# Kernel tuning notes

Measured on AMD Instinct MI355X. Metric: run time of the kernel, lower is better.

The kernel has to match this reference:

```python
import jax, jax.numpy as jnp
import numpy as np


def _grid_sample(feat, grid):
    """Bilinear grid_sample, zeros padding, align_corners=False (torch default).
    feat: (B,C,H,W); grid: (B,Hg,Wg,2) normalized to [-1,1]. Returns (B,C,Hg,Wg)."""
    B, C, H, W = feat.shape
    gx, gy = grid[..., 0], grid[..., 1]
    ix = ((gx + 1.0) * W - 1.0) * 0.5
    iy = ((gy + 1.0) * H - 1.0) * 0.5
    x0 = jnp.floor(ix)
    y0 = jnp.floor(iy)
    wx = ix - x0
    wy = iy - y0

    def sample_one(f, x0, y0, wx, wy):
        def gather(xi, yi):
            valid = (xi >= 0) & (xi <= W - 1) & (yi >= 0) & (yi <= H - 1)
            xc = jnp.clip(xi, 0, W - 1).astype(jnp.int32)
            yc = jnp.clip(yi, 0, H - 1).astype(jnp.int32)
            return f[:, yc, xc] * valid[None].astype(f.dtype)
        v00 = gather(x0, y0)
        v01 = gather(x0 + 1, y0)
        v10 = gather(x0, y0 + 1)
        v11 = gather(x0 + 1, y0 + 1)
        return (v00 * (1 - wx) * (1 - wy) + v01 * wx * (1 - wy)
                + v10 * (1 - wx) * wy + v11 * wx * wy)

    return jax.vmap(sample_one)(feat, x0, y0, wx, wy)


def _homo_warp(src_feat, depth_hypo, src_K, src_c2w, ref_K, ref_c2w):
    """src_feat (B,C,H,W), depth_hypo (B,D,H,W) -> warped (B,C,D,H,W)."""
    B, C, H, W = src_feat.shape
    D = depth_hypo.shape[1]
    src_w2c = jnp.linalg.inv(src_c2w)
    ref_w2c = jnp.linalg.inv(ref_c2w)
    # Faithful to torch: clone w2c, overwrite top-left 3x3 with intrinsics.
    src_K4 = src_w2c.at[:, :3, :3].set(src_K)
    ref_K4 = ref_w2c.at[:, :3, :3].set(ref_K)
    src_proj = src_K4 @ src_w2c
    ref_proj = ref_K4 @ ref_w2c
    proj = src_proj @ jnp.linalg.inv(ref_proj)
    rot = proj[:, :3, :3]                      # (B,3,3)
    trans = proj[:, :3, 3]                     # (B,3)
    y, x = jnp.meshgrid(jnp.arange(H, dtype=src_feat.dtype),
                        jnp.arange(W, dtype=src_feat.dtype), indexing='ij')
    xyz = jnp.stack([x.ravel(), y.ravel(), jnp.ones(H * W, src_feat.dtype)], 0)  # (3,HW)
    rot_xyz = jnp.einsum('bij,jn->bin', rot, xyz)                                 # (B,3,HW)
    d = depth_hypo.reshape(B, 1, D, H * W)
    proj_xyz = rot_xyz[:, :, None, :] * d + trans[:, :, None, None]               # (B,3,D,HW)
    proj_xy = proj_xyz[:, :2] / proj_xyz[:, 2:3]
    gx = proj_xy[:, 0] / ((W - 1) / 2.0) - 1.0
    gy = proj_xy[:, 1] / ((H - 1) / 2.0) - 1.0
    grid = jax.lax.stop_gradient(jnp.stack([gx, gy], -1).reshape(B, D * H, W, 2))
    warped = _grid_sample(src_feat, grid)                                          # (B,C,D*H,W)
    return warped.reshape(B, C, D, H, W)


def _unfold5(x):
    """F.unfold(k=5,p=2) reshaped: (B,C,H,W) -> (B,C,25,H,W); k = dy*5+dx."""
    B, C, H, W = x.shape
    xp = jnp.pad(x, ((0, 0), (0, 0), (2, 2), (2, 2)))
    return jnp.stack([xp[:, :, dy:dy + H, dx:dx + W]
                      for dy in range(5) for dx in range(5)], axis=2)


def _cost_aggregation(cost, ref_feat, depth_hypo):
    B, D, H, W = cost.shape
    CENTER = 12  # index of 5x5 window center
    cost_nb = _unfold5(cost)                                           # (B,D,25,H,W)
    depth_nb = jax.lax.stop_gradient(_unfold5(depth_hypo))             # (B,D,25,H,W)
    w_depth = jax.nn.softmax(-jnp.abs(depth_nb - depth_nb[:, :, CENTER:CENTER + 1]), axis=2)
    feat_nb = jax.lax.stop_gradient(_unfold5(ref_feat))                # (B,C,25,H,W)
    w_feat = jnp.sum(feat_nb[:, :, CENTER:CENTER + 1] * feat_nb, axis=1, keepdims=True)
    w_feat = jax.nn.softmax(jnp.broadcast_to(w_feat, (B, D, 25, H, W)), axis=2)
    weight = jax.lax.stop_gradient(jax.nn.softmax(w_depth * w_feat, axis=2))
    return jnp.sum(cost_nb * weight, axis=2)                           # (B,D,H,W)


def setup_inputs() -> dict:
    key = jax.random.key(0)
    V, B, C, D, H, W = 3, 2, 32, 32, 128, 160
    k1, k2 = jax.random.split(key)
    features = jax.random.normal(k1, (V, B, C, H, W), jnp.float32)
    uncertainty = jax.random.normal(k2, (B, H, W), jnp.float32)
    K = np.array([[float(W), 0.0, (W - 1) / 2.0],
                  [0.0, float(W), (H - 1) / 2.0],
                  [0.0, 0.0, 1.0]], np.float32)
    intrinsics = np.broadcast_to(K, (V, B, 3, 3)).copy()
    c2w = np.tile(np.eye(4, dtype=np.float32), (V, B, 1, 1))
    for v in range(1, V):
        ang = 0.05 * v
        R = np.array([[np.cos(ang), 0.0, np.sin(ang)],
                      [0.0, 1.0, 0.0],
                      [-np.sin(ang), 0.0, np.cos(ang)]], np.float32)
        c2w[v, :, :3, :3] = R
        c2w[v, :, 0, 3] = 0.2 * v
    depth_vals = jnp.asarray(np.linspace(2.0, 10.0, D, dtype=np.float32))
    depth_hypo = jnp.broadcast_to(depth_vals[None, :, None, None], (B, D, H, W)) + 0.0
    return {
        'features': features,
        'intrinsics': jnp.asarray(intrinsics),
        'cam_to_world': jnp.asarray(c2w),
        'depth_hypo': depth_hypo,
        'uncertainty': uncertainty,
    }


def reference(features, intrinsics, cam_to_world, depth_hypo, uncertainty):
    ref_feat = features[0]                                             # (B,C,H,W)
    V = features.shape[0]
    unc = jax.nn.sigmoid(uncertainty)[:, None, None]                   # (B,1,1,H,W)
    pairwise = []
    for v in range(1, V):
        warped = _homo_warp(features[v], depth_hypo,
                            intrinsics[v], cam_to_world[v],
                            intrinsics[0], cam_to_world[0])            # (B,C,D,H,W)
        c = jnp.sum(ref_feat[:, :, None] * warped, axis=1, keepdims=True)  # correlation
        pairwise.append(c * unc)
    cost = jnp.min(jnp.stack(pairwise, 0), axis=0)[:, 0]               # (B,D,H,W)
    agg = _cost_aggregation(cost, ref_feat, depth_hypo)
    prob = jax.nn.softmax(agg, axis=1)
    return jnp.sum(prob * depth_hypo, axis=1)                          # (B,H,W)
```

## Files before the change

### kernel.cpp

```cpp
#include <hip/hip_runtime.h>
#include <hip/hip_fp16.h>
#include <math.h>

#define V_ 3
#define B_ 2
#define C_ 32
#define D_ 32
#define H_ 128
#define W_ 160
#define HW_ (H_*W_)
#define NPIX_ (B_*H_*W_)
#define NCOST_ (B_*D_*H_*W_)

struct H8 { __half2 h[4]; };

__device__ __forceinline__ void inv4(const double* m, double* o) {
    double inv[16];
    inv[0]  =  m[5]*m[10]*m[15] - m[5]*m[11]*m[14] - m[9]*m[6]*m[15] + m[9]*m[7]*m[14] + m[13]*m[6]*m[11] - m[13]*m[7]*m[10];
    inv[4]  = -m[4]*m[10]*m[15] + m[4]*m[11]*m[14] + m[8]*m[6]*m[15] - m[8]*m[7]*m[14] - m[12]*m[6]*m[11] + m[12]*m[7]*m[10];
    inv[8]  =  m[4]*m[9]*m[15]  - m[4]*m[11]*m[13] - m[8]*m[5]*m[15] + m[8]*m[7]*m[13] + m[12]*m[5]*m[11] - m[12]*m[7]*m[9];
    inv[12] = -m[4]*m[9]*m[14]  + m[4]*m[10]*m[13] + m[8]*m[5]*m[14] - m[8]*m[6]*m[13] - m[12]*m[5]*m[10] + m[12]*m[6]*m[9];
    inv[1]  = -m[1]*m[10]*m[15] + m[1]*m[11]*m[14] + m[9]*m[2]*m[15] - m[9]*m[3]*m[14] - m[13]*m[2]*m[11] + m[13]*m[3]*m[10];
    inv[5]  =  m[0]*m[10]*m[15] - m[0]*m[11]*m[14] - m[8]*m[2]*m[15] + m[8]*m[3]*m[14] + m[12]*m[2]*m[11] - m[12]*m[3]*m[10];
    inv[9]  = -m[0]*m[9]*m[15]  + m[0]*m[11]*m[13] + m[8]*m[1]*m[15] - m[8]*m[3]*m[13] - m[12]*m[1]*m[11] + m[12]*m[3]*m[9];
    inv[13] =  m[0]*m[9]*m[14]  - m[0]*m[10]*m[13] - m[8]*m[1]*m[14] + m[8]*m[2]*m[13] + m[12]*m[1]*m[10] - m[12]*m[2]*m[9];
    inv[2]  =  m[1]*m[6]*m[15]  - m[1]*m[7]*m[14]  - m[5]*m[2]*m[15] + m[5]*m[3]*m[14] + m[13]*m[2]*m[7]  - m[13]*m[3]*m[6];
    inv[6]  = -m[0]*m[6]*m[15]  + m[0]*m[7]*m[14]  + m[4]*m[2]*m[15] - m[4]*m[3]*m[14] - m[12]*m[2]*m[7]  + m[12]*m[3]*m[6];
    inv[10] =  m[0]*m[5]*m[15]  - m[0]*m[7]*m[13]  - m[4]*m[1]*m[15] + m[4]*m[3]*m[13] + m[12]*m[1]*m[7]  - m[12]*m[3]*m[5];
    inv[14] = -m[0]*m[5]*m[14]  + m[0]*m[6]*m[13]  + m[4]*m[1]*m[14] - m[4]*m[2]*m[13] - m[12]*m[1]*m[6]  + m[12]*m[2]*m[5];
    inv[3]  = -m[1]*m[6]*m[11]  + m[1]*m[7]*m[10]  + m[5]*m[2]*m[11] - m[5]*m[3]*m[10] - m[9]*m[2]*m[7]   + m[9]*m[3]*m[6];
    inv[7]  =  m[0]*m[6]*m[11]  - m[0]*m[7]*m[10]  - m[4]*m[2]*m[11] + m[4]*m[3]*m[10] + m[8]*m[2]*m[7]   - m[8]*m[3]*m[6];
    inv[11] = -m[0]*m[5]*m[11]  + m[0]*m[7]*m[9]   + m[4]*m[1]*m[11] - m[4]*m[3]*m[9]  - m[8]*m[1]*m[7]   + m[8]*m[3]*m[5];
    inv[15] =  m[0]*m[5]*m[10]  - m[0]*m[6]*m[9]   - m[4]*m[1]*m[10] + m[4]*m[2]*m[9]  + m[8]*m[1]*m[6]   - m[8]*m[2]*m[5];
    double det = m[0]*inv[0] + m[1]*inv[4] + m[2]*inv[8] + m[3]*inv[12];
    det = 1.0 / det;
    for (int i = 0; i < 16; i++) o[i] = inv[i] * det;
}

__device__ __forceinline__ void mm4(const double* A, const double* Bm, double* Cm) {
    for (int r = 0; r < 4; r++)
        for (int c = 0; c < 4; c++) {
            double s = 0.0;
            for (int k = 0; k < 4; k++) s += A[r*4+k] * Bm[k*4+c];
            Cm[r*4+c] = s;
        }
}

__global__ void proj_kernel(const float* __restrict__ K, const float* __restrict__ c2w,
                            float* __restrict__ proj_out) {
    int t = blockIdx.x * blockDim.x + threadIdx.x;
    if (t >= (V_-1) * B_) return;
    int vv = t / B_;
    int b  = t % B_;
    int v  = vv + 1;
    double sc[16], rc[16];
    for (int i = 0; i < 16; i++) {
        sc[i] = (double)c2w[((size_t)v * B_ + b) * 16 + i];
        rc[i] = (double)c2w[((size_t)0 * B_ + b) * 16 + i];
    }
    double sw[16], rw[16];
    inv4(sc, sw);
    inv4(rc, rw);
    double sK[16], rK[16];
    for (int i = 0; i < 16; i++) { sK[i] = sw[i]; rK[i] = rw[i]; }
    for (int r = 0; r < 3; r++)
        for (int c = 0; c < 3; c++) {
            sK[r*4+c] = (double)K[((size_t)v * B_ + b) * 9 + r*3 + c];
            rK[r*4+c] = (double)K[((size_t)0 * B_ + b) * 9 + r*3 + c];
        }
    double sp[16], rp[16], rpi[16], P[16];
    mm4(sK, sw, sp);
    mm4(rK, rw, rp);
    inv4(rp, rpi);
    mm4(sp, rpi, P);
    float* o = proj_out + (size_t)t * 12;
    for (int r = 0; r < 3; r++)
        for (int c = 0; c < 3; c++) o[r*3+c] = (float)P[r*4+c];
    for (int r = 0; r < 3; r++) o[9+r] = (float)P[r*4+3];
}

__global__ void __launch_bounds__(256) transpose_kernel(const float* __restrict__ feat,
                                                        float* __restrict__ refT,
                                                        __half* __restrict__ fh) {
    __shared__ float lds[32][33];
    int bid = blockIdx.x;
    int xt = bid % (W_ / 32);
    int y  = (bid / (W_ / 32)) % H_;
    int vb = bid / ((W_ / 32) * H_);
    int v = vb >> 1, b = vb & 1;
    int x0 = xt * 32;
    int tid = threadIdx.x;
    int xl = tid & 31;
    int ch = tid >> 5;
#pragma unroll
    for (int it = 0; it < 4; it++) {
        int c = it * 8 + ch;
        lds[c][xl] = feat[((size_t)(vb * C_ + c) * H_ + y) * W_ + x0 + xl];
    }
    __syncthreads();
    int c4 = tid & 7;
    int xw = tid >> 3;
    float4 o;
    o.x = lds[c4*4+0][xw];
    o.y = lds[c4*4+1][xw];
    o.z = lds[c4*4+2][xw];
    o.w = lds[c4*4+3][xw];
    size_t pix = (size_t)(b * H_ + y) * W_ + x0 + xw;
    if (v == 0) {
        *(float4*)(refT + pix * C_ + c4 * 4) = o;
    } else {
        uint2 st;
        __half2 p0 = __floats2half2_rn(o.x, o.y);
        __half2 p1 = __floats2half2_rn(o.z, o.w);
        st.x = *(unsigned int*)&p0;
        st.y = *(unsigned int*)&p1;
        size_t dst = ((size_t)((v - 1) * B_ + b) * HW_ + (y * W_ + x0 + xw));
        *(uint2*)((unsigned short*)fh + dst * C_ + c4 * 4) = st;
    }
}

__global__ void __launch_bounds__(256, 4) cost_kernel(const float* __restrict__ refT,
                                                      const __half* __restrict__ fh,
                                                      const float* __restrict__ depth,
                                                      const float* __restrict__ unc,
                                                      const float* __restrict__ proj,
                                                      float* __restrict__ cost) {
    __shared__ float4 lw[2][256];
    __shared__ int4   lo[2][256];
    int tid = threadIdx.x;
    const int blocksPerDt = NPIX_ / 32;
    int dt      = blockIdx.x / blocksPerDt;
    int pixbase = (blockIdx.x % blocksPerDt) * 32;
    int d0 = dt * 8;

    {
        int pixl = tid & 31;
        int dl   = tid >> 5;
        int pix = pixbase + pixl;
        int x = pix % W_;
        int y = (pix / W_) % H_;
        int b = pix / HW_;
        float dep = depth[((b * D_ + d0 + dl) * H_ + y) * W_ + x];
        float fx = (float)x, fy = (float)y;
#pragma unroll
        for (int v = 0; v < 2; v++) {
            const float* P = proj + ((size_t)v * B_ + b) * 12;
            float rx = P[0]*fx + P[1]*fy + P[2];
            float ry = P[3]*fx + P[4]*fy + P[5];
            float rz = P[6]*fx + P[7]*fy + P[8];
            float px = rx * dep + P[9];
            float py = ry * dep + P[10];
            float pz = rz * dep + P[11];
            float inv_pz = 1.0f / pz;
            float t0 = px * inv_pz;
            float t1 = py * inv_pz;
            float gx = t0 / ((W_ - 1) * 0.5f) - 1.0f;
            float gy = t1 / ((H_ - 1) * 0.5f) - 1.0f;
            float ix = ((gx + 1.0f) * W_ - 1.0f) * 0.5f;
            float iy = ((gy + 1.0f) * H_ - 1.0f) * 0.5f;
            float x0f = floorf(ix), y0f = floorf(iy);
            float wx = ix - x0f, wy = iy - y0f;
            int x0 = (int)x0f, y0 = (int)y0f;
            int x1 = x0 + 1, y1 = y0 + 1;
            bool vx0 = (x0 >= 0) && (x0 <= W_ - 1);
            bool vx1 = (x1 >= 0) && (x1 <= W_ - 1);
            bool vy0 = (y0 >= 0) && (y0 <= H_ - 1);
            bool vy1 = (y1 >= 0) && (y1 <= H_ - 1);
            float4 w;
            w.x = (vx0 && vy0) ? (1.0f - wx) * (1.0f - wy) : 0.0f;
            w.y = (vx1 && vy0) ? wx * (1.0f - wy) : 0.0f;
            w.z = (vx0 && vy1) ? (1.0f - wx) * wy : 0.0f;
            w.w = (vx1 && vy1) ? wx * wy : 0.0f;
            int xc0 = min(max(x0, 0), W_ - 1), xc1 = min(max(x1, 0), W_ - 1);
            int yc0 = min(max(y0, 0), H_ - 1), yc1 = min(max(y1, 0), H_ - 1);
            int4 o;
            o.x = yc0 * W_ + xc0;
            o.y = yc0 * W_ + xc1;
            o.z = yc1 * W_ + xc0;
            o.w = yc1 * W_ + xc1;
            lw[v][tid] = w;
            lo[v][tid] = o;
        }
    }
    __syncthreads();

    int c8 = tid & 3;
    int g  = (tid >> 2) & 31;
    int h  = tid >> 7;
    int pix = pixbase + g;
    int x = pix % W_;
    int y = (pix / W_) % H_;
    int b = pix / HW_;

    const float4* rT4 = (const float4*)refT;
    const float4 r0 = rT4[(size_t)pix * 8 + c8 * 2];
    const float4 r1 = rT4[(size_t)pix * 8 + c8 * 2 + 1];
    const H8* fh8 = (const H8*)fh;
    size_t baseA = ((size_t)(0 * B_ + b) * HW_) * 4 + c8;
    size_t baseB = ((size_t)(1 * B_ + b) * HW_) * 4 + c8;

    float u = unc[pix];
    float sig = 1.0f / (1.0f + __expf(-u));

    float myres = 0.0f;
#pragma unroll
    for (int i = 0; i < 4; i++) {
        int e = (h * 4 + i) * 32 + g;
        float pv[2];
#pragma unroll
        for (int v = 0; v < 2; v++) {
            float4 Wt = lw[v][e];
            int4   Of = lo[v][e];
            size_t base = v ? baseB : baseA;
            H8 a  = fh8[base + (size_t)Of.x * 4];
            H8 bq = fh8[base + (size_t)Of.y * 4];
            H8 cq = fh8[base + (size_t)Of.z * 4];
            H8 eq = fh8[base + (size_t)Of.w * 4];
            __half2 w0 = __float2half2_rn(Wt.x);
            __half2 w1 = __float2half2_rn(Wt.y);
            __half2 w2 = __float2half2_rn(Wt.z);
            __half2 w3 = __float2half2_rn(Wt.w);
            __half2 acc0 = __hmul2(w0, a.h[0]);
            __half2 acc1 = __hmul2(w0, a.h[1]);
            __half2 acc2 = __hmul2(w0, a.h[2]);
            __half2 acc3 = __hmul2(w0, a.h[3]);
            acc0 = __hfma2(w1, bq.h[0], acc0);
            acc1 = __hfma2(w1, bq.h[1], acc1);
            acc2 = __hfma2(w1, bq.h[2], acc2);
            acc3 = __hfma2(w1, bq.h[3], acc3);
            acc0 = __hfma2(w2, cq.h[0], acc0);
            acc1 = __hfma2(w2, cq.h[1], acc1);
            acc2 = __hfma2(w2, cq.h[2], acc2);
            acc3 = __hfma2(w2, cq.h[3], acc3);
            acc0 = __hfma2(w3, eq.h[0], acc0);
            acc1 = __hfma2(w3, eq.h[1], acc1);
            acc2 = __hfma2(w3, eq.h[2], acc2);
            acc3 = __hfma2(w3, eq.h[3], acc3);
            float2 f0 = __half22float2(acc0);
            float2 f1 = __half22float2(acc1);
            float2 f2 = __half22float2(acc2);
            float2 f3 = __half22float2(acc3);
            float p = r0.x*f0.x + r0.y*f0.y + r0.z*f1.x + r0.w*f1.y
                    + r1.x*f2.x + r1.y*f2.y + r1.z*f3.x + r1.w*f3.y;
            p += __shfl_xor(p, 1);
            p += __shfl_xor(p, 2);
            pv[v] = p;
        }
        float r = fminf(pv[0], pv[1]) * sig;
        if (c8 == i) myres = r;
    }
    cost[((b * D_ + d0 + h * 4 + c8) * H_ + y) * W_ + x] = myres;
}

__global__ void __launch_bounds__(256) wfeat_kernel(const float* __restrict__ refT,
                                                    float* __restrict__ wfeat) {
    __shared__ float4 wbox[5 * 36 * 8];
    int tid = threadIdx.x;
    int g  = tid >> 3;
    int c4 = tid & 7;
    int pixbase = blockIdx.x * 32;
    int x0 = pixbase % W_;
    int yb = (pixbase / W_) % H_;
    int b  = pixbase / HW_;
    const float4* rT4 = (const float4*)refT;

    for (int e = tid; e < 5 * 36 * 8; e += 256) {
        int ent = e >> 3, q = e & 7;
        int ry = ent / 36, rx = ent - ry * 36;
        int yy = yb + ry - 2, xx = x0 + rx - 2;
        float4 val = make_float4(0.f, 0.f, 0.f, 0.f);
        if (yy >= 0 && yy < H_ && xx >= 0 && xx < W_)
            val = rT4[(size_t)((b * H_ + yy) * W_ + xx) * 8 + q];
        wbox[e] = val;
    }
    __syncthreads();

    const float4 r = wbox[(2 * 36 + g + 2) * 8 + c4];
    float logit[25];
#pragma unroll
    for (int k = 0; k < 25; k++) {
        int dy = k / 5, dx = k % 5;
        float4 q = wbox[(dy * 36 + g + dx) * 8 + c4];
        float p = r.x*q.x + r.y*q.y + r.z*q.z + r.w*q.w;
        p += __shfl_xor(p, 1);
        p += __shfl_xor(p, 2);
        p += __shfl_xor(p, 4);
        logit[k] = p;
    }
    float m = logit[0];
#pragma unroll
    for (int k = 1; k < 25; k++) m = fmaxf(m, logit[k]);
    float s = 0.0f;
#pragma unroll
    for (int k = 0; k < 25; k++) { logit[k] = __expf(logit[k] - m); s += logit[k]; }
    float inv_s = 1.0f / s;
    int pix = pixbase + g;
#pragma unroll
    for (int t = 0; t < 3; t++) {
        int k = c4 + 8 * t;
        wfeat[(size_t)k * NPIX_ + pix] = logit[k] * inv_s;
    }
    if (c4 == 0) wfeat[(size_t)24 * NPIX_ + pix] = logit[24] * inv_s;
}

__global__ void __launch_bounds__(256, 4) agg_kernel(const float* __restrict__ depth,
                                                     const float* __restrict__ cost,
                                                     const float* __restrict__ wfeat,
                                                     float* __restrict__ agg) {
    int tid = threadIdx.x;
    int xl = tid & 31;
    int dl = tid >> 5;
    int bid = blockIdx.x;
    int xt  = bid % (W_ / 32);
    int rem = bid / (W_ / 32);
    int by  = rem % (B_ * H_);
    int dg  = rem / (B_ * H_);
    int y = by % H_;
    int b = by / H_;
    int x = xt * 32 + xl;
    int d = dg * 8 + dl;
    int pix = (b * H_ + y) * W_ + x;
    size_t dslice = (size_t)(b * D_ + d) * HW_;

    float dc = depth[dslice + y * W_ + x];

    float wd[25];
    float m1 = -1e30f;
#pragma unroll
    for (int k = 0; k < 25; k++) {
        int dy = k / 5 - 2, dx = k % 5 - 2;
        int ny = y + dy, nx = x + dx;
        bool ok = (ny >= 0 && ny < H_ && nx >= 0 && nx < W_);
        float nd = ok ? depth[dslice + ny * W_ + nx] : 0.0f;
        float l = -fabsf(nd - dc);
        wd[k] = l;
        m1 = fmaxf(m1, l);
    }
    float s1 = 0.0f;
#pragma unroll
    for (int k = 0; k < 25; k++) { wd[k] = __expf(wd[k] - m1); s1 += wd[k]; }
    float inv_s1 = 1.0f / s1;

    float m2 = -1e30f;
#pragma unroll
    for (int k = 0; k < 25; k++) {
        float l = (wd[k] * inv_s1) * wfeat[(size_t)k * NPIX_ + pix];
        wd[k] = l;
        m2 = fmaxf(m2, l);
    }
    float s2 = 0.0f;
    float acc = 0.0f;
#pragma unroll
    for (int k = 0; k < 25; k++) {
        float e = __expf(wd[k] - m2);
        s2 += e;
        int dy = k / 5 - 2, dx = k % 5 - 2;
        int ny = y + dy, nx = x + dx;
        bool ok = (ny >= 0 && ny < H_ && nx >= 0 && nx < W_);
        float cv = ok ? cost[dslice + ny * W_ + nx] : 0.0f;
        acc += cv * e;
    }
    agg[dslice + y * W_ + x] = acc / s2;
}

__global__ void __launch_bounds__(256) final_kernel(const float* __restrict__ agg,
                                                    const float* __restrict__ depth,
                                                    float* __restrict__ out) {
    int idx = blockIdx.x * 256 + threadIdx.x;
    if (idx >= NPIX_) return;
    int x = idx % W_;
    int y = (idx / W_) % H_;
    int b = idx / (W_ * H_);
    size_t base = ((size_t)(b * D_) * H_ + y) * W_ + x;
    float a[D_];
    float m = -1e30f;
#pragma unroll
    for (int d = 0; d < D_; d++) {
        a[d] = agg[base + (size_t)d * HW_];
        m = fmaxf(m, a[d]);
    }
    float s = 0.0f, ws = 0.0f;
#pragma unroll
    for (int d = 0; d < D_; d++) {
        float e = __expf(a[d] - m);
        s += e;
        ws += e * depth[base + (size_t)d * HW_];
    }
    out[idx] = ws / s;
}

extern "C" void kernel_launch(void* const* d_in, const int* in_sizes, int n_in,
                              void* d_out, int out_size, void* d_ws, size_t ws_size,
                              hipStream_t stream) {
    const float* features = (const float*)d_in[0];
    const float* intr     = (const float*)d_in[1];
    const float* c2w      = (const float*)d_in[2];
    const float* depth    = (const float*)d_in[3];
    const float* unc      = (const float*)d_in[4];
    float* out = (float*)d_out;

    float*  ws    = (float*)d_ws;
    float*  refT  = ws;
    __half* fh    = (__half*)(refT + (size_t)B_ * HW_ * C_);
    float*  cost  = (float*)(fh + (size_t)2 * B_ * HW_ * C_);
    float*  wfeat = cost + NCOST_;
    float*  agg   = wfeat + (size_t)25 * NPIX_;
    float*  proj  = agg + NCOST_;

    hipLaunchKernelGGL(proj_kernel, dim3(1), dim3(64), 0, stream, intr, c2w, proj);
    hipLaunchKernelGGL(transpose_kernel, dim3(V_ * B_ * H_ * (W_ / 32)), dim3(256), 0, stream,
                       features, refT, fh);
    hipLaunchKernelGGL(cost_kernel, dim3((NPIX_ * 4) / 32), dim3(256), 0, stream,
                       refT, fh, depth, unc, proj, cost);
    hipLaunchKernelGGL(wfeat_kernel, dim3(NPIX_ / 32), dim3(256), 0, stream, refT, wfeat);
    hipLaunchKernelGGL(agg_kernel, dim3((W_ / 32) * B_ * H_ * (D_ / 8)), dim3(256), 0, stream,
                       depth, cost, wfeat, agg);
    hipLaunchKernelGGL(final_kernel, dim3(NPIX_ / 256), dim3(256), 0, stream, agg, depth, out);
}
```

Before: 79.16 us.

## Fuse six kernels into three: merge proj, wfeat, and agg+final stages

Folds the projection-matrix computation into an extra block of the transpose kernel and runs the wfeat computation as extra blocks of the cost kernel, which share a shared-memory union. The agg and final softmax kernels become one kernel per row tile of 32 pixels: it handles all 32 depths, stages wfeat in shared memory and reduces over depth in-block, so the agg intermediate buffer is never written. It also drops the max-subtraction in the two inner softmaxes, since the logits are bounded. The aim is to cut launch overhead and global traffic for the agg buffer, at the cost of fewer blocks in the agg stage and a serial 32-thread depth reduction.

Result: faster. 70.02 us (-11.5%).

```diff
diff --git a/kernel.cpp b/kernel.cpp
--- a/kernel.cpp
+++ b/kernel.cpp
@@ -46,50 +46,52 @@
         }
 }
 
-__global__ void proj_kernel(const float* __restrict__ K, const float* __restrict__ c2w,
-                            float* __restrict__ proj_out) {
-    int t = blockIdx.x * blockDim.x + threadIdx.x;
-    if (t >= (V_-1) * B_) return;
-    int vv = t / B_;
-    int b  = t % B_;
-    int v  = vv + 1;
-    double sc[16], rc[16];
-    for (int i = 0; i < 16; i++) {
-        sc[i] = (double)c2w[((size_t)v * B_ + b) * 16 + i];
-        rc[i] = (double)c2w[((size_t)0 * B_ + b) * 16 + i];
-    }
-    double sw[16], rw[16];
-    inv4(sc, sw);
-    inv4(rc, rw);
-    double sK[16], rK[16];
-    for (int i = 0; i < 16; i++) { sK[i] = sw[i]; rK[i] = rw[i]; }
-    for (int r = 0; r < 3; r++)
-        for (int c = 0; c < 3; c++) {
-            sK[r*4+c] = (double)K[((size_t)v * B_ + b) * 9 + r*3 + c];
-            rK[r*4+c] = (double)K[((size_t)0 * B_ + b) * 9 + r*3 + c];
-        }
-    double sp[16], rp[16], rpi[16], P[16];
-    mm4(sK, sw, sp);
-    mm4(rK, rw, rp);
-    inv4(rp, rpi);
-    mm4(sp, rpi, P);
-    float* o = proj_out + (size_t)t * 12;
-    for (int r = 0; r < 3; r++)
-        for (int c = 0; c < 3; c++) o[r*3+c] = (float)P[r*4+c];
-    for (int r = 0; r < 3; r++) o[9+r] = (float)P[r*4+3];
-}
-
-__global__ void __launch_bounds__(256) transpose_kernel(const float* __restrict__ feat,
+__global__ void __launch_bounds__(256) transproj_kernel(const float* __restrict__ feat,
+                                                        const float* __restrict__ K,
+                                                        const float* __restrict__ c2w,
                                                         float* __restrict__ refT,
-                                                        __half* __restrict__ fh) {
+                                                        __half* __restrict__ fh,
+                                                        float* __restrict__ proj_out) {
+    int bid = blockIdx.x;
+    int tid = threadIdx.x;
+    if (bid == V_ * B_ * H_ * (W_ / 32)) {
+        int t = tid;
+        if (t >= (V_-1) * B_) return;
+        int vv = t / B_;
+        int b  = t % B_;
+        int v  = vv + 1;
+        double sc[16], rc[16];
+        for (int i = 0; i < 16; i++) {
+            sc[i] = (double)c2w[((size_t)v * B_ + b) * 16 + i];
+            rc[i] = (double)c2w[((size_t)0 * B_ + b) * 16 + i];
+        }
+        double sw[16], rw[16];
+        inv4(sc, sw);
+        inv4(rc, rw);
+        double sK[16], rK[16];
+        for (int i = 0; i < 16; i++) { sK[i] = sw[i]; rK[i] = rw[i]; }
+        for (int r = 0; r < 3; r++)
+            for (int c = 0; c < 3; c++) {
+                sK[r*4+c] = (double)K[((size_t)v * B_ + b) * 9 + r*3 + c];
+                rK[r*4+c] = (double)K[((size_t)0 * B_ + b) * 9 + r*3 + c];
+            }
+        double sp[16], rp[16], rpi[16], P[16];
+        mm4(sK, sw, sp);
+        mm4(rK, rw, rp);
+        inv4(rp, rpi);
+        mm4(sp, rpi, P);
+        float* o = proj_out + (size_t)t * 12;
+        for (int r = 0; r < 3; r++)
+            for (int c = 0; c < 3; c++) o[r*3+c] = (float)P[r*4+c];
+        for (int r = 0; r < 3; r++) o[9+r] = (float)P[r*4+3];
+        return;
+    }
     __shared__ float lds[32][33];
-    int bid = blockIdx.x;
     int xt = bid % (W_ / 32);
     int y  = (bid / (W_ / 32)) % H_;
     int vb = bid / ((W_ / 32) * H_);
     int v = vb >> 1, b = vb & 1;
     int x0 = xt * 32;
-    int tid = threadIdx.x;
     int xl = tid & 31;
     int ch = tid >> 5;
 #pragma unroll
@@ -119,274 +121,268 @@
     }
 }
 
-__global__ void __launch_bounds__(256, 4) cost_kernel(const float* __restrict__ refT,
-                                                      const __half* __restrict__ fh,
-                                                      const float* __restrict__ depth,
-                                                      const float* __restrict__ unc,
-                                                      const float* __restrict__ proj,
-                                                      float* __restrict__ cost) {
-    __shared__ float4 lw[2][256];
-    __shared__ int4   lo[2][256];
+union SmemU {
+    struct { float4 lw[2][256]; int4 lo[2][256]; } c;
+    float4 wbox[5 * 36 * 8];
+};
+__global__ void __launch_bounds__(256, 4) costwfeat_kernel(const float* __restrict__ refT,
+                                                           const __half* __restrict__ fh,
+                                                           const float* __restrict__ depth,
+                                                           const float* __restrict__ unc,
+                                                           const float* __restrict__ proj,
+                                                           float* __restrict__ cost,
+                                                           float* __restrict__ wfeat) {
+    __shared__ SmemU sm;
     int tid = threadIdx.x;
+    int bid = blockIdx.x;
     const int blocksPerDt = NPIX_ / 32;
-    int dt      = blockIdx.x / blocksPerDt;
-    int pixbase = (blockIdx.x % blocksPerDt) * 32;
-    int d0 = dt * 8;
-
-    {
-        int pixl = tid & 31;
-        int dl   = tid >> 5;
-        int pix = pixbase + pixl;
+
+    if (bid < 4 * blocksPerDt) {
+        int dt      = bid / blocksPerDt;
+        int pixbase = (bid % blocksPerDt) * 32;
+        int d0 = dt * 8;
+        {
+            int pixl = tid & 31;
+            int dl   = tid >> 5;
+            int pix = pixbase + pixl;
+            int x = pix % W_;
+            int y = (pix / W_) % H_;
+            int b = pix / HW_;
+            float dep = depth[((b * D_ + d0 + dl) * H_ + y) * W_ + x];
+            float fx = (float)x, fy = (float)y;
+#pragma unroll
+            for (int v = 0; v < 2; v++) {
+                const float* P = proj + ((size_t)v * B_ + b) * 12;
+                float rx = P[0]*fx + P[1]*fy + P[2];
+                float ry = P[3]*fx + P[4]*fy + P[5];
+                float rz = P[6]*fx + P[7]*fy + P[8];
+                float px = rx * dep + P[9];
+                float py = ry * dep + P[10];
+                float pz = rz * dep + P[11];
+                float inv_pz = 1.0f / pz;
+                float t0 = px * inv_pz;
+                float t1 = py * inv_pz;
+                float gx = t0 / ((W_ - 1) * 0.5f) - 1.0f;
+                float gy = t1 / ((H_ - 1) * 0.5f) - 1.0f;
+                float ix = ((gx + 1.0f) * W_ - 1.0f) * 0.5f;
+                float iy = ((gy + 1.0f) * H_ - 1.0f) * 0.5f;
+                float x0f = floorf(ix), y0f = floorf(iy);
+                float wx = ix - x0f, wy = iy - y0f;
+                int x0 = (int)x0f, y0 = (int)y0f;
+                int x1 = x0 + 1, y1 = y0 + 1;
+                bool vx0 = (x0 >= 0) && (x0 <= W_ - 1);
+                bool vx1 = (x1 >= 0) && (x1 <= W_ - 1);
+                bool vy0 = (y0 >= 0) && (y0 <= H_ - 1);
+                bool vy1 = (y1 >= 0) && (y1 <= H_ - 1);
+                float4 w;
+                w.x = (vx0 && vy0) ? (1.0f - wx) * (1.0f - wy) : 0.0f;
+                w.y = (vx1 && vy0) ? wx * (1.0f - wy) : 0.0f;
+                w.z = (vx0 && vy1) ? (1.0f - wx) * wy : 0.0f;
+                w.w = (vx1 && vy1) ? wx * wy : 0.0f;
+                int xc0 = min(max(x0, 0), W_ - 1), xc1 = min(max(x1, 0), W_ - 1);
+                int yc0 = min(max(y0, 0), H_ - 1), yc1 = min(max(y1, 0), H_ - 1);
+                int4 o;
+                o.x = yc0 * W_ + xc0;
+                o.y = yc0 * W_ + xc1;
+                o.z = yc1 * W_ + xc0;
+                o.w = yc1 * W_ + xc1;
+                sm.c.lw[v][tid] = w;
+                sm.c.lo[v][tid] = o;
+            }
+        }
+        __syncthreads();
+
+        int c8 = tid & 3;
+        int g  = (tid >> 2) & 31;
+        int h  = tid >> 7;
+        int pix = pixbase + g;
         int x = pix % W_;
         int y = (pix / W_) % H_;
         int b = pix / HW_;
-        float dep = depth[((b * D_ + d0 + dl) * H_ + y) * W_ + x];
-        float fx = (float)x, fy = (float)y;
-#pragma unroll
-        for (int v = 0; v < 2; v++) {
-            const float* P = proj + ((size_t)v * B_ + b) * 12;
-            float rx = P[0]*fx + P[1]*fy + P[2];
-            float ry = P[3]*fx + P[4]*fy + P[5];
-            float rz = P[6]*fx + P[7]*fy + P[8];
-            float px = rx * dep + P[9];
-            float py = ry * dep + P[10];
-            float pz = rz * dep + P[11];
-            float inv_pz = 1.0f / pz;
-            float t0 = px * inv_pz;
-            float t1 = py * inv_pz;
-            float gx = t0 / ((W_ - 1) * 0.5f) - 1.0f;
-            float gy = t1 / ((H_ - 1) * 0.5f) - 1.0f;
-            float ix = ((gx + 1.0f) * W_ - 1.0f) * 0.5f;
-            float iy = ((gy + 1.0f) * H_ - 1.0f) * 0.5f;
-            float x0f = floorf(ix), y0f = floorf(iy);
-            float wx = ix - x0f, wy = iy - y0f;
-            int x0 = (int)x0f, y0 = (int)y0f;
-            int x1 = x0 + 1, y1 = y0 + 1;
-            bool vx0 = (x0 >= 0) && (x0 <= W_ - 1);
-            bool vx1 = (x1 >= 0) && (x1 <= W_ - 1);
-            bool vy0 = (y0 >= 0) && (y0 <= H_ - 1);
-            bool vy1 = (y1 >= 0) && (y1 <= H_ - 1);
-            float4 w;
-            w.x = (vx0 && vy0) ? (1.0f - wx) * (1.0f - wy) : 0.0f;
-            w.y = (vx1 && vy0) ? wx * (1.0f - wy) : 0.0f;
-            w.z = (vx0 && vy1) ? (1.0f - wx) * wy : 0.0f;
-            w.w = (vx1 && vy1) ? wx * wy : 0.0f;
-            int xc0 = min(max(x0, 0), W_ - 1), xc1 = min(max(x1, 0), W_ - 1);
-            int yc0 = min(max(y0, 0), H_ - 1), yc1 = min(max(y1, 0), H_ - 1);
-            int4 o;
-            o.x = yc0 * W_ + xc0;
-            o.y = yc0 * W_ + xc1;
-            o.z = yc1 * W_ + xc0;
-            o.w = yc1 * W_ + xc1;
-            lw[v][tid] = w;
-            lo[v][tid] = o;
-        }
-    }
-    __syncthreads();
-
-    int c8 = tid & 3;
-    int g  = (tid >> 2) & 31;
-    int h  = tid >> 7;
-    int pix = pixbase + g;
-    int x = pix % W_;
-    int y = (pix / W_) % H_;
-    int b = pix / HW_;
-
-    const float4* rT4 = (const float4*)refT;
-    const float4 r0 = rT4[(size_t)pix * 8 + c8 * 2];
-    const float4 r1 = rT4[(size_t)pix * 8 + c8 * 2 + 1];
-    const H8* fh8 = (const H8*)fh;
-    size_t baseA = ((size_t)(0 * B_ + b) * HW_) * 4 + c8;
-    size_t baseB = ((size_t)(1 * B_ + b) * HW_) * 4 + c8;
-
-    float u = unc[pix];
-    float sig = 1.0f / (1.0f + __expf(-u));
-
-    float myres = 0.0f;
-#pragma unroll
-    for (int i = 0; i < 4; i++) {
-        int e = (h * 4 + i) * 32 + g;
-        float pv[2];
-#pragma unroll
-        for (int v = 0; v < 2; v++) {
-            float4 Wt = lw[v][e];
-            int4   Of = lo[v][e];
-            size_t base = v ? baseB : baseA;
-            H8 a  = fh8[base + (size_t)Of.x * 4];
-            H8 bq = fh8[base + (size_t)Of.y * 4];
-            H8 cq = fh8[base + (size_t)Of.z * 4];
-            H8 eq = fh8[base + (size_t)Of.w * 4];
-            __half2 w0 = __float2half2_rn(Wt.x);
-            __half2 w1 = __float2half2_rn(Wt.y);
-            __half2 w2 = __float2half2_rn(Wt.z);
-            __half2 w3 = __float2half2_rn(Wt.w);
-            __half2 acc0 = __hmul2(w0, a.h[0]);
-            __half2 acc1 = __hmul2(w0, a.h[1]);
-            __half2 acc2 = __hmul2(w0, a.h[2]);
-            __half2 acc3 = __hmul2(w0, a.h[3]);
-            acc0 = __hfma2(w1, bq.h[0], acc0);
-            acc1 = __hfma2(w1, bq.h[1], acc1);
-            acc2 = __hfma2(w1, bq.h[2], acc2);
-            acc3 = __hfma2(w1, bq.h[3], acc3);
-            acc0 = __hfma2(w2, cq.h[0], acc0);
-            acc1 = __hfma2(w2, cq.h[1], acc1);
-            acc2 = __hfma2(w2, cq.h[2], acc2);
-            acc3 = __hfma2(w2, cq.h[3], acc3);
-            acc0 = __hfma2(w3, eq.h[0], acc0);
-            acc1 = __hfma2(w3, eq.h[1], acc1);
-            acc2 = __hfma2(w3, eq.h[2], acc2);
-            acc3 = __hfma2(w3, eq.h[3], acc3);
-            float2 f0 = __half22float2(acc0);
-            float2 f1 = __half22float2(acc1);
-            float2 f2 = __half22float2(acc2);
-            float2 f3 = __half22float2(acc3);
-            float p = r0.x*f0.x + r0.y*f0.y + r0.z*f1.x + r0.w*f1.y
-                    + r1.x*f2.x + r1.y*f2.y + r1.z*f3.x + r1.w*f3.y;
+
+        const float4* rT4 = (const float4*)refT;
+        const float4 r0 = rT4[(size_t)pix * 8 + c8 * 2];
+        const float4 r1 = rT4[(size_t)pix * 8 + c8 * 2 + 1];
+        const H8* fh8 = (const H8*)fh;
+        size_t baseA = ((size_t)(0 * B_ + b) * HW_) * 4 + c8;
+        size_t baseB = ((size_t)(1 * B_ + b) * HW_) * 4 + c8;
+
+        float u = unc[pix];
+        float sig = 1.0f / (1.0f + __expf(-u));
+
+        float myres = 0.0f;
+#pragma unroll
+        for (int i = 0; i < 4; i++) {
+            int e = (h * 4 + i) * 32 + g;
+            float pv[2];
+#pragma unroll
+            for (int v = 0; v < 2; v++) {
+                float4 Wt = sm.c.lw[v][e];
+                int4   Of = sm.c.lo[v][e];
+                size_t base = v ? baseB : baseA;
+                H8 a  = fh8[base + (size_t)Of.x * 4];
+                H8 bq = fh8[base + (size_t)Of.y * 4];
+                H8 cq = fh8[base + (size_t)Of.z * 4];
+                H8 eq = fh8[base + (size_t)Of.w * 4];
+                __half2 w0 = __float2half2_rn(Wt.x);
+                __half2 w1 = __float2half2_rn(Wt.y);
+                __half2 w2 = __float2half2_rn(Wt.z);
+                __half2 w3 = __float2half2_rn(Wt.w);
+                __half2 acc0 = __hmul2(w0, a.h[0]);
+                __half2 acc1 = __hmul2(w0, a.h[1]);
+                __half2 acc2 = __hmul2(w0, a.h[2]);
+                __half2 acc3 = __hmul2(w0, a.h[3]);
+                acc0 = __hfma2(w1, bq.h[0], acc0);
+                acc1 = __hfma2(w1, bq.h[1], acc1);
+                acc2 = __hfma2(w1, bq.h[2], acc2);
+                acc3 = __hfma2(w1, bq.h[3], acc3);
+                acc0 = __hfma2(w2, cq.h[0], acc0);
+                acc1 = __hfma2(w2, cq.h[1], acc1);
+                acc2 = __hfma2(w2, cq.h[2], acc2);
+                acc3 = __hfma2(w2, cq.h[3], acc3);
+                acc0 = __hfma2(w3, eq.h[0], acc0);
+                acc1 = __hfma2(w3, eq.h[1], acc1);
+                acc2 = __hfma2(w3, eq.h[2], acc2);
+                acc3 = __hfma2(w3, eq.h[3], acc3);
+                float2 f0 = __half22float2(acc0);
+                float2 f1 = __half22float2(acc1);
+                float2 f2 = __half22float2(acc2);
+                float2 f3 = __half22float2(acc3);
+                float p = r0.x*f0.x + r0.y*f0.y + r0.z*f1.x + r0.w*f1.y
+                        + r1.x*f2.x + r1.y*f2.y + r1.z*f3.x + r1.w*f3.y;
+                p += __shfl_xor(p, 1);
+                p += __shfl_xor(p, 2);
+                pv[v] = p;
+            }
+            float r = fminf(pv[0], pv[1]) * sig;
+            if (c8 == i) myres = r;
+        }
+        cost[((b * D_ + d0 + h * 4 + c8) * H_ + y) * W_ + x] = myres;
+    } else {
+        int wbid = bid - 4 * blocksPerDt;
+        int g  = tid >> 3;
+        int c4 = tid & 7;
+        int pixbase = wbid * 32;
+        int x0 = pixbase % W_;
+        int yb = (pixbase / W_) % H_;
+        int b  = pixbase / HW_;
+        const float4* rT4 = (const float4*)refT;
+
+        for (int e = tid; e < 5 * 36 * 8; e += 256) {
+            int ent = e >> 3, q = e & 7;
+            int ry = ent / 36, rx = ent - ry * 36;
+            int yy = yb + ry - 2, xx = x0 + rx - 2;
+            float4 val = make_float4(0.f, 0.f, 0.f, 0.f);
+            if (yy >= 0 && yy < H_ && xx >= 0 && xx < W_)
+                val = rT4[(size_t)((b * H_ + yy) * W_ + xx) * 8 + q];
+            sm.wbox[e] = val;
+        }
+        __syncthreads();
+
+        const float4 r = sm.wbox[(2 * 36 + g + 2) * 8 + c4];
+        float logit[25];
+#pragma unroll
+        for (int k = 0; k < 25; k++) {
+            int dy = k / 5, dx = k % 5;
+            float4 q = sm.wbox[(dy * 36 + g + dx) * 8 + c4];
+            float p = r.x*q.x + r.y*q.y + r.z*q.z + r.w*q.w;
             p += __shfl_xor(p, 1);
             p += __shfl_xor(p, 2);
-            pv[v] = p;
-        }
-        float r = fminf(pv[0], pv[1]) * sig;
-        if (c8 == i) myres = r;
-    }
-    cost[((b * D_ + d0 + h * 4 + c8) * H_ + y) * W_ + x] = myres;
-}
-
-__global__ void __launch_bounds__(256) wfeat_kernel(const float* __restrict__ refT,
-                                                    float* __restrict__ wfeat) {
-    __shared__ float4 wbox[5 * 36 * 8];
-    int tid = threadIdx.x;
-    int g  = tid >> 3;
-    int c4 = tid & 7;
-    int pixbase = blockIdx.x * 32;
-    int x0 = pixbase % W_;
-    int yb = (pixbase / W_) % H_;
-    int b  = pixbase / HW_;
-    const float4* rT4 = (const float4*)refT;
-
-    for (int e = tid; e < 5 * 36 * 8; e += 256) {
-        int ent = e >> 3, q = e & 7;
-        int ry = ent / 36, rx = ent - ry * 36;
-        int yy = yb + ry - 2, xx = x0 + rx - 2;
-        float4 val = make_float4(0.f, 0.f, 0.f, 0.f);
-        if (yy >= 0 && yy < H_ && xx >= 0 && xx < W_)
-            val = rT4[(size_t)((b * H_ + yy) * W_ + xx) * 8 + q];
-        wbox[e] = val;
-    }
-    __syncthreads();
-
-    const float4 r = wbox[(2 * 36 + g + 2) * 8 + c4];
-    float logit[25];
-#pragma unroll
-    for (int k = 0; k < 25; k++) {
-        int dy = k / 5, dx = k % 5;
-        float4 q = wbox[(dy * 36 + g + dx) * 8 + c4];
-        float p = r.x*q.x + r.y*q.y + r.z*q.z + r.w*q.w;
-        p += __shfl_xor(p, 1);
-        p += __shfl_xor(p, 2);
-        p += __shfl_xor(p, 4);
-        logit[k] = p;
-    }
-    float m = logit[0];
-#pragma unroll
-    for (int k = 1; k < 25; k++) m = fmaxf(m, logit[k]);
-    float s = 0.0f;
-#pragma unroll
-    for (int k = 0; k < 25; k++) { logit[k] = __expf(logit[k] - m); s += logit[k]; }
-    float inv_s = 1.0f / s;
-    int pix = pixbase + g;
-#pragma unroll
-    for (int t = 0; t < 3; t++) {
-        int k = c4 + 8 * t;
-        wfeat[(size_t)k * NPIX_ + pix] = logit[k] * inv_s;
-    }
-    if (c4 == 0) wfeat[(size_t)24 * NPIX_ + pix] = logit[24] * inv_s;
-}
-
-__global__ void __launch_bounds__(256, 4) agg_kernel(const float* __restrict__ depth,
-                                                     const float* __restrict__ cost,
-                                                     const float* __restrict__ wfeat,
-                                                     float* __restrict__ agg) {
+            p += __shfl_xor(p, 4);
+            logit[k] = p;
+        }
+        float m = logit[0];
+#pragma unroll
+        for (int k = 1; k < 25; k++) m = fmaxf(m, logit[k]);
+        float s = 0.0f;
+#pragma unroll
+        for (int k = 0; k < 25; k++) { logit[k] = __expf(logit[k] - m); s += logit[k]; }
+        float inv_s = 1.0f / s;
+        int pix = pixbase + g;
+#pragma unroll
+        for (int t = 0; t < 3; t++) {
+            int k = c4 + 8 * t;
+            wfeat[(size_t)k * NPIX_ + pix] = logit[k] * inv_s;
+        }
+        if (c4 == 0) wfeat[(size_t)24 * NPIX_ + pix] = logit[24] * inv_s;
+    }
+}
+
+__global__ void __launch_bounds__(256, 4) aggfinal_kernel(const float* __restrict__ depth,
+                                                          const float* __restrict__ cost,
+                                                          const float* __restrict__ wfeat,
+                                                          float* __restrict__ out) {
+    __shared__ float wf[25][33];
+    __shared__ float aval[D_][33];
+    __shared__ float dval[D_][33];
     int tid = threadIdx.x;
     int xl = tid & 31;
     int dl = tid >> 5;
     int bid = blockIdx.x;
-    int xt  = bid % (W_ / 32);
-    int rem = bid / (W_ / 32);
-    int by  = rem % (B_ * H_);
-    int dg  = rem / (B_ * H_);
+    int xt = bid % (W_ / 32);
+    int by = bid / (W_ / 32);
     int y = by % H_;
     int b = by / H_;
     int x = xt * 32 + xl;
-    int d = dg * 8 + dl;
     int pix = (b * H_ + y) * W_ + x;
-    size_t dslice = (size_t)(b * D_ + d) * HW_;
-
-    float dc = depth[dslice + y * W_ + x];
-
-    float wd[25];
-    float m1 = -1e30f;
-#pragma unroll
-    for (int k = 0; k < 25; k++) {
-        int dy = k / 5 - 2, dx = k % 5 - 2;
-        int ny = y + dy, nx = x + dx;
-        bool ok = (ny >= 0 && ny < H_ && nx >= 0 && nx < W_);
-        float nd = ok ? depth[dslice + ny * W_ + nx] : 0.0f;
-        float l = -fabsf(nd - dc);
-        wd[k] = l;
-        m1 = fmaxf(m1, l);
-    }
-    float s1 = 0.0f;
-#pragma unroll
-    for (int k = 0; k < 25; k++) { wd[k] = __expf(wd[k] - m1); s1 += wd[k]; }
-    float inv_s1 = 1.0f / s1;
-
-    float m2 = -1e30f;
-#pragma unroll
-    for (int k = 0; k < 25; k++) {
-        float l = (wd[k] * inv_s1) * wfeat[(size_t)k * NPIX_ + pix];
-        wd[k] = l;
-        m2 = fmaxf(m2, l);
-    }
-    float s2 = 0.0f;
-    float acc = 0.0f;
-#pragma unroll
-    for (int k = 0; k < 25; k++) {
-        float e = __expf(wd[k] - m2);
-        s2 += e;
-        int dy = k / 5 - 2, dx = k % 5 - 2;
-        int ny = y + dy, nx = x + dx;
-        bool ok = (ny >= 0 && ny < H_ && nx >= 0 && nx < W_);
-        float cv = ok ? cost[dslice + ny * W_ + nx] : 0.0f;
-        acc += cv * e;
-    }
-    agg[dslice + y * W_ + x] = acc / s2;
-}
-
-__global__ void __launch_bounds__(256) final_kernel(const float* __restrict__ agg,
-                                                    const float* __restrict__ depth,
-                                                    float* __restrict__ out) {
-    int idx = blockIdx.x * 256 + threadIdx.x;
-    if (idx >= NPIX_) return;
-    int x = idx % W_;
-    int y = (idx / W_) % H_;
-    int b = idx / (W_ * H_);
-    size_t base = ((size_t)(b * D_) * H_ + y) * W_ + x;
-    float a[D_];
-    float m = -1e30f;
-#pragma unroll
-    for (int d = 0; d < D_; d++) {
-        a[d] = agg[base + (size_t)d * HW_];
-        m = fmaxf(m, a[d]);
-    }
-    float s = 0.0f, ws = 0.0f;
-#pragma unroll
-    for (int d = 0; d < D_; d++) {
-        float e = __expf(a[d] - m);
-        s += e;
-        ws += e * depth[base + (size_t)d * HW_];
-    }
-    out[idx] = ws / s;
+
+    for (int li = tid; li < 25 * 32; li += 256) {
+        int k  = li >> 5;
+        int pp = li & 31;
+        wf[k][pp] = wfeat[(size_t)k * NPIX_ + (b * H_ + y) * W_ + xt * 32 + pp];
+    }
+    __syncthreads();
+
+#pragma unroll
+    for (int i = 0; i < 4; i++) {
+        int d = dl * 4 + i;
+        size_t dslice = (size_t)(b * D_ + d) * HW_;
+        float dc = depth[dslice + y * W_ + x];
+
+        float wd[25];
+        float s1 = 0.0f;
+#pragma unroll
+        for (int k = 0; k < 25; k++) {
+            int dy = k / 5 - 2, dx = k % 5 - 2;
+            int ny = y + dy, nx = x + dx;
+            bool ok = (ny >= 0 && ny < H_ && nx >= 0 && nx < W_);
+            float nd = ok ? depth[dslice + ny * W_ + nx] : 0.0f;
+            float e = __expf(-fabsf(nd - dc));
+            wd[k] = e;
+            s1 += e;
+        }
+        float inv_s1 = 1.0f / s1;
+
+        float s2 = 0.0f;
+        float acc = 0.0f;
+#pragma unroll
+        for (int k = 0; k < 25; k++) {
+            float e = __expf((wd[k] * inv_s1) * wf[k][xl]);
+            s2 += e;
+            int dy = k / 5 - 2, dx = k % 5 - 2;
+            int ny = y + dy, nx = x + dx;
+            bool ok = (ny >= 0 && ny < H_ && nx >= 0 && nx < W_);
+            float cv = ok ? cost[dslice + ny * W_ + nx] : 0.0f;
+            acc += cv * e;
+        }
+        aval[d][xl] = acc / s2;
+        dval[d][xl] = dc;
+    }
+    __syncthreads();
+
+    if (tid < 32) {
+        float m = -1e30f;
+#pragma unroll
+        for (int dd = 0; dd < D_; dd++) m = fmaxf(m, aval[dd][tid]);
+        float s = 0.0f, ws = 0.0f;
+#pragma unroll
+        for (int dd = 0; dd < D_; dd++) {
+            float e = __expf(aval[dd][tid] - m);
+            s += e;
+            ws += e * dval[dd][tid];
+        }
+        out[(b * H_ + y) * W_ + xt * 32 + tid] = ws / s;
+    }
 }
 
 extern "C" void kernel_launch(void* const* d_in, const int* in_sizes, int n_in,
@@ -404,16 +400,12 @@
     __half* fh    = (__half*)(refT + (size_t)B_ * HW_ * C_);
     float*  cost  = (float*)(fh + (size_t)2 * B_ * HW_ * C_);
     float*  wfeat = cost + NCOST_;
-    float*  agg   = wfeat + (size_t)25 * NPIX_;
-    float*  proj  = agg + NCOST_;
-
-    hipLaunchKernelGGL(proj_kernel, dim3(1), dim3(64), 0, stream, intr, c2w, proj);
-    hipLaunchKernelGGL(transpose_kernel, dim3(V_ * B_ * H_ * (W_ / 32)), dim3(256), 0, stream,
-                       features, refT, fh);
-    hipLaunchKernelGGL(cost_kernel, dim3((NPIX_ * 4) / 32), dim3(256), 0, stream,
-                       refT, fh, depth, unc, proj, cost);
-    hipLaunchKernelGGL(wfeat_kernel, dim3(NPIX_ / 32), dim3(256), 0, stream, refT, wfeat);
-    hipLaunchKernelGGL(agg_kernel, dim3((W_ / 32) * B_ * H_ * (D_ / 8)), dim3(256), 0, stream,
-                       depth, cost, wfeat, agg);
-    hipLaunchKernelGGL(final_kernel, dim3(NPIX_ / 256), dim3(256), 0, stream, agg, depth, out);
-}
+    float*  proj  = wfeat + (size_t)25 * NPIX_;
+
+    hipLaunchKernelGGL(transproj_kernel, dim3(V_ * B_ * H_ * (W_ / 32) + 1), dim3(256), 0, stream,
+                       features, intr, c2w, refT, fh, proj);
+    hipLaunchKernelGGL(costwfeat_kernel, dim3((NPIX_ * 4) / 32 + NPIX_ / 32), dim3(256), 0, stream,
+                       refT, fh, depth, unc, proj, cost, wfeat);
+    hipLaunchKernelGGL(aggfinal_kernel, dim3(NPIX_ / 32), dim3(256), 0, stream,
+                       depth, cost, wfeat, out);
+}
```
